# Kernel optimization log

Hardware: AMD Instinct MI355X
Metric: run time of the kernel (lower is better)

Reference implementation:

```python
import jax, jax.numpy as jnp
import numpy as np

EMB = 1024
HEADS = 16
HEAD_DIM = EMB // HEADS
SCALE = 1.0 / np.sqrt(HEAD_DIM)


def setup_inputs() -> dict:
    key = jax.random.key(0)
    ks = jax.random.split(key, 11)
    B, L, E = 4, 2048, EMB
    s = 1.0 / np.sqrt(E)
    inp = {
        "Q": jax.random.normal(ks[0], (B, L, E), jnp.float32),
        "K": jax.random.normal(ks[1], (B, L, E), jnp.float32),
        "V": jax.random.normal(ks[2], (B, L, E), jnp.float32),
        "WQ": jax.random.normal(ks[3], (E, E), jnp.float32) * s,
        "bQ": jax.random.normal(ks[4], (E,), jnp.float32) * s,
        "WK": jax.random.normal(ks[5], (E, E), jnp.float32) * s,
        "bK": jax.random.normal(ks[6], (E,), jnp.float32) * s,
        "WV": jax.random.normal(ks[7], (E, E), jnp.float32) * s,
        "bV": jax.random.normal(ks[8], (E,), jnp.float32) * s,
        "WO": jax.random.normal(ks[9], (E, E), jnp.float32) * s,
        "bO": jax.random.normal(ks[10], (E,), jnp.float32) * s,
    }
    return inp


def reference(Q, K, V, WQ, bQ, WK, bK, WV, bV, WO, bO):
    B, L, E = Q.shape
    # linear projections (torch Linear stores W as [out,in]; here W is [in,out])
    q = Q @ WQ + bQ
    k = K @ WK + bK
    v = V @ WV + bV
    # split heads: [B, H, L, D]
    q = q.reshape(B, L, HEADS, HEAD_DIM).transpose(0, 2, 1, 3)
    k = k.reshape(B, L, HEADS, HEAD_DIM).transpose(0, 2, 1, 3)
    v = v.reshape(B, L, HEADS, HEAD_DIM).transpose(0, 2, 1, 3)
    scores = jnp.einsum("bhqd,bhkd->bhqk", q, k) * SCALE
    # causal mask (mask=True): -inf above diagonal
    causal = jnp.tril(jnp.ones((L, L), dtype=bool))
    scores = jnp.where(causal, scores, -jnp.inf)
    probs = jax.nn.softmax(scores, axis=-1)
    out = jnp.einsum("bhqk,bhkd->bhqd", probs, v)  # [B,H,L,D]
    out = out.transpose(0, 2, 1, 3).reshape(B, L, E)  # concat heads
    return out @ WO + bO
```

## Files before the change

### kernel.cpp

```cpp
#include <hip/hip_runtime.h>
#include <hip/hip_bf16.h>

#define BB 4
#define HH 16
#define LL 2048
#define DD 64
#define EE 1024
#define MM (BB*LL)
#define SCL 0.125f
#define L2E 1.44269504f

using bf16   = __hip_bfloat16;
using bf16x8 = __attribute__((ext_vector_type(8))) __bf16;
using s16x4  = __attribute__((ext_vector_type(4))) short;
using f32x4  = __attribute__((ext_vector_type(4))) float;
using u32x4  = __attribute__((ext_vector_type(4))) unsigned int;
typedef unsigned int u32;

__device__ __forceinline__ bf16x8 ld8(const bf16* p){ return *(const bf16x8*)p; }
__device__ __forceinline__ bf16x8 ld8(const float* p){
  u32x4 a = *(const u32x4*)p;
  u32x4 b = *(const u32x4*)(p + 4);
  union { bf16x8 v; unsigned short s[8]; } r;
#pragma unroll
  for (int i = 0; i < 4; i++) r.s[i]     = (unsigned short)((a[i] + 0x7FFFu + ((a[i] >> 16) & 1u)) >> 16);
#pragma unroll
  for (int i = 0; i < 4; i++) r.s[i + 4] = (unsigned short)((b[i] + 0x7FFFu + ((b[i] >> 16) & 1u)) >> 16);
  return r.v;
}
__device__ __forceinline__ float ldf(const bf16* p){ return __bfloat162float(*p); }
__device__ __forceinline__ float ldf(const float* p){ return *p; }
__device__ __forceinline__ bf16 to_b(bf16 v){ return v; }
__device__ __forceinline__ bf16 to_b(float v){ return __float2bfloat16(v); }

__device__ __forceinline__ void async16(const bf16* g, bf16* l) {
  __builtin_amdgcn_global_load_lds((const __attribute__((address_space(1))) u32*)g,
                                   (__attribute__((address_space(3))) u32*)l, 16, 0, 0);
}

__global__ __launch_bounds__(256) void detect_dtype(const unsigned int* __restrict__ w,
                                                    int* __restrict__ flag) {
  __shared__ int cnt[256];
  int tid = threadIdx.x;
  int c = 0;
  for (int i = 0; i < 16; i++) {
    unsigned u = w[tid * 16 + i];
    unsigned e = (u >> 7) & 0xFF;
    c += (e >= 100 && e <= 140) ? 1 : 0;
  }
  cnt[tid] = c;
  __syncthreads();
  for (int s = 128; s > 0; s >>= 1) {
    if (tid < s) cnt[tid] += cnt[tid + s];
    __syncthreads();
  }
  if (tid == 0) *flag = (cnt[0] > 2048) ? 1 : 0;
}

__global__ __launch_bounds__(256) void convert_in(
    const void* __restrict__ X0, const void* __restrict__ X1, const void* __restrict__ X2,
    bf16* __restrict__ Y0, bf16* __restrict__ Y1, bf16* __restrict__ Y2,
    const int* __restrict__ flag) {
  int z = blockIdx.z;
  const void* X = (z == 0) ? X0 : (z == 1) ? X1 : X2;
  bf16* Y       = (z == 0) ? Y0 : (z == 1) ? Y1 : Y2;
  size_t idx = ((size_t)blockIdx.x * 256 + threadIdx.x) * 8;
  if (*flag) *(bf16x8*)(Y + idx) = *(const bf16x8*)((const bf16*)X + idx);
  else       *(bf16x8*)(Y + idx) = ld8((const float*)X + idx);
}

template<typename T>
__device__ __forceinline__ void tr_body(const T* __restrict__ W, bf16* __restrict__ Wt,
                                        bf16 (*t)[33]) {
  int tx = threadIdx.x, ty = threadIdx.y;
  int x = blockIdx.x * 32 + tx;
  for (int r = 0; r < 4; r++)
    t[ty + r * 8][tx] = to_b(W[(blockIdx.y * 32 + ty + r * 8) * EE + x]);
  __syncthreads();
  int x2 = blockIdx.y * 32 + tx;
  for (int r = 0; r < 4; r++)
    Wt[(blockIdx.x * 32 + ty + r * 8) * EE + x2] = t[tx][ty + r * 8];
}

__global__ __launch_bounds__(256) void transpose_w4(
    const void* __restrict__ W0, const void* __restrict__ W1,
    const void* __restrict__ W2, const void* __restrict__ W3,
    bf16* __restrict__ T0, bf16* __restrict__ T1,
    bf16* __restrict__ T2, bf16* __restrict__ T3,
    const int* __restrict__ flag) {
  __shared__ bf16 t[32][33];
  int z = blockIdx.z;
  const void* W = (z == 0) ? W0 : (z == 1) ? W1 : (z == 2) ? W2 : W3;
  bf16* Wt      = (z == 0) ? T0 : (z == 1) ? T1 : (z == 2) ? T2 : T3;
  if (*flag) tr_body<bf16>((const bf16*)W, Wt, t);
  else       tr_body<float>((const float*)W, Wt, t);
}

#define TILE_ELEMS (128 * 64)
template<typename TIO>
__device__ void gemm_body(const bf16* __restrict__ A, const bf16* __restrict__ Bt,
                          const TIO* __restrict__ bias, void* __restrict__ Cv,
                          int mode, bf16* As, bf16* Bs) {
  constexpr int K = EE;
  int tid = threadIdx.x;
  int lane = tid & 63, w = tid >> 6;
  int l16 = lane & 15, quad = lane >> 4;
  int linear = blockIdx.x + 8 * blockIdx.y;
  int xcd = linear & 7;
  int slot = linear >> 3;
  int m0 = (xcd * 8 + (slot & 7)) * 128;
  int n0 = (slot >> 3) * 128;
  int mw = (w & 1) * 64;
  int nw = (w >> 1) * 64;
  int lr = lane >> 3;
  int x7 = l16 & 7;

  f32x4 acc[4][4] = {};

  auto stage = [&](bf16* Ad, bf16* Bd, int k0) {
#pragma unroll
    for (int s = 0; s < 4; s++) {
      int R = w * 32 + s * 8;
      int r = R + lr;
      int gc = ((lane & 7) ^ (r & 7)) * 8;
      async16(A  + (size_t)(m0 + r) * K + k0 + gc, Ad + R * 64);
      async16(Bt + (size_t)(n0 + r) * K + k0 + gc, Bd + R * 64);
    }
  };

  auto compute = [&](const bf16* Ab, const bf16* Bb) {
#pragma unroll
    for (int ks = 0; ks < 2; ks++) {
      bf16x8 af[4], bfr[4];
#pragma unroll
      for (int t = 0; t < 4; t++) {
        af[t]  = *(const bf16x8*)(Ab + (mw + t * 16 + l16) * 64 + ((ks * 4 + quad) ^ x7) * 8);
        bfr[t] = *(const bf16x8*)(Bb + (nw + t * 16 + l16) * 64 + ((ks * 4 + quad) ^ x7) * 8);
      }
#pragma unroll
      for (int mt = 0; mt < 4; mt++)
#pragma unroll
        for (int nt = 0; nt < 4; nt++)
          acc[mt][nt] = __builtin_amdgcn_mfma_f32_16x16x32_bf16(af[mt], bfr[nt], acc[mt][nt], 0, 0, 0);
    }
  };

  stage(As, Bs, 0);
  asm volatile("s_waitcnt vmcnt(0)" ::: "memory");
  __builtin_amdgcn_s_barrier();
  asm volatile("" ::: "memory");

#pragma unroll 1
  for (int t = 0; t < K / 64; t += 2) {
    stage(As + TILE_ELEMS, Bs + TILE_ELEMS, t * 64 + 64);
    compute(As, Bs);
    asm volatile("s_waitcnt vmcnt(0)" ::: "memory");
    __builtin_amdgcn_s_barrier();
    asm volatile("" ::: "memory");
    if (t + 2 < K / 64)
      stage(As, Bs, t * 64 + 128);
    compute(As + TILE_ELEMS, Bs + TILE_ELEMS);
    asm volatile("s_waitcnt vmcnt(0)" ::: "memory");
    __builtin_amdgcn_s_barrier();
    asm volatile("" ::: "memory");
  }

#pragma unroll
  for (int nt = 0; nt < 4; nt++) {
    int col = n0 + nw + nt * 16 + l16;
    float bv = ldf(bias + col);
    int hh = col >> 6, d = col & 63;
#pragma unroll
    for (int mt = 0; mt < 4; mt++) {
      f32x4 v = acc[mt][nt];
      int rowb = m0 + mw + mt * 16 + quad * 4;
      if (mode == 0) {
#pragma unroll
        for (int i = 0; i < 4; i++)
          ((bf16*)Cv)[(size_t)(rowb + i) * EE + col] = __float2bfloat16(v[i] + bv);
      } else if (mode == 3) {
#pragma unroll
        for (int i = 0; i < 4; i++) {
          float val = v[i] + bv;
          if constexpr (__is_same(TIO, bf16))
            ((bf16*)Cv)[(size_t)(rowb + i) * EE + col] = __float2bfloat16(val);
          else
            ((float*)Cv)[(size_t)(rowb + i) * EE + col] = val;
        }
      } else {
        int b = rowb >> 11, l0 = rowb & 2047;
        union { s16x4 p; bf16 e[4]; } u;
#pragma unroll
        for (int i = 0; i < 4; i++) u.e[i] = __float2bfloat16(v[i] + bv);
        *(s16x4*)((bf16*)Cv + ((size_t)(b * HH + hh) * DD + d) * LL + l0) = u.p;
      }
    }
  }
}

__global__ __launch_bounds__(256) void qkv_gemm(
    const bf16* __restrict__ Qc, const bf16* __restrict__ Kc, const bf16* __restrict__ Vc,
    const bf16* __restrict__ WQt, const bf16* __restrict__ WKt, const bf16* __restrict__ WVt,
    const void* __restrict__ bQ, const void* __restrict__ bK, const void* __restrict__ bV,
    bf16* __restrict__ qo, bf16* __restrict__ ko, bf16* __restrict__ vo,
    const int* __restrict__ flag) {
  __shared__ __align__(16) bf16 As[2 * TILE_ELEMS];
  __shared__ __align__(16) bf16 Bs[2 * TILE_ELEMS];
  int z = blockIdx.z;
  const bf16* A    = (z == 0) ? Qc  : (z == 1) ? Kc  : Vc;
  const bf16* Bt   = (z == 0) ? WQt : (z == 1) ? WKt : WVt;
  const void* bb   = (z == 0) ? bQ  : (z == 1) ? bK  : bV;
  bf16* C          = (z == 0) ? qo  : (z == 1) ? ko  : vo;
  int mode = (z == 2) ? 2 : 0;
  if (*flag) gemm_body<bf16>(A, Bt, (const bf16*)bb, C, mode, As, Bs);
  else       gemm_body<float>(A, Bt, (const float*)bb, C, mode, As, Bs);
}

__global__ __launch_bounds__(256) void out_gemm(const bf16* __restrict__ A,
                                                const bf16* __restrict__ WOt,
                                                const void* __restrict__ bO,
                                                void* __restrict__ C,
                                                const int* __restrict__ flag) {
  __shared__ __align__(16) bf16 As[2 * TILE_ELEMS];
  __shared__ __align__(16) bf16 Bs[2 * TILE_ELEMS];
  if (*flag) gemm_body<bf16>(A, WOt, (const bf16*)bO, C, 3, As, Bs);
  else       gemm_body<float>(A, WOt, (const float*)bO, C, 3, As, Bs);
}

__global__ __launch_bounds__(256) void attn(const bf16* __restrict__ qg,
                                            const bf16* __restrict__ kg,
                                            const bf16* __restrict__ vg,
                                            bf16* __restrict__ outg) {
  __shared__ __align__(16) bf16 Ks[2][64 * 64];
  __shared__ __align__(16) bf16 Vs[2][64 * 64];
  int linear = blockIdx.x + 16 * blockIdx.y;
  int xcd = linear & 7;
  int slot = linear >> 3;
  int bh = xcd * 8 + (slot & 7);
  int pb = slot >> 3;
  int tid = threadIdx.x;
  int w = tid >> 6, lane = tid & 63, l16 = lane & 15, quad = lane >> 4;
  int b = bh >> 4, hh = bh & 15;

  const bf16* qp = qg + (size_t)b * LL * EE + hh * DD;
  const bf16* kp = kg + (size_t)b * LL * EE + hh * DD;
  const bf16* vp = vg + (size_t)bh * DD * LL;
  const f32x4 z4 = {};
  int x7 = l16 & 7;

  for (int half = 0; half < 2; half++) {
    int tile = half ? (31 - pb) : pb;
    int qrow0 = tile * 64 + w * 16;
    int q = qrow0 + l16;
    bf16x8 bq0 = *(const bf16x8*)(qp + (size_t)q * EE + quad * 8);
    bf16x8 bq1 = *(const bf16x8*)(qp + (size_t)q * EE + 32 + quad * 8);

    float m = -1.0e30f, l = 0.f;
    f32x4 o[4] = {};
    int kend = tile + 1;

    __syncthreads();
    {
      int kbase = 0;
#pragma unroll
      for (int t = 0; t < 2; t++) {
        int R = w * 16 + t * 8;
        int r = R + (lane >> 3);
        int gb = (lane & 7) ^ (r & 7);
        async16(kp + (size_t)(kbase + r) * EE + gb * 8, &Ks[0][R * 64]);
        async16(vp + (size_t)r * LL + kbase + gb * 8, &Vs[0][R * 64]);
      }
    }

    for (int kb = 0; kb < kend; kb++) {
      int kbase = kb * 64;
      __syncthreads();
      if (kb + 1 < kend) {
        int nb = (kb + 1) & 1;
        int nbase = kbase + 64;
#pragma unroll
        for (int t = 0; t < 2; t++) {
          int R = w * 16 + t * 8;
          int r = R + (lane >> 3);
          int gb = (lane & 7) ^ (r & 7);
          async16(kp + (size_t)(nbase + r) * EE + gb * 8, &Ks[nb][R * 64]);
          async16(vp + (size_t)r * LL + nbase + gb * 8, &Vs[nb][R * 64]);
        }
      }
      const bf16* Kb = &Ks[kb & 1][0];
      const bf16* Vb = &Vs[kb & 1][0];

      f32x4 s[4];
      __builtin_amdgcn_s_setprio(1);
#pragma unroll
      for (int kt = 0; kt < 4; kt++) {
        int row = kt * 16 + l16;
        bf16x8 kf0 = *(const bf16x8*)(Kb + row * 64 + (quad ^ x7) * 8);
        bf16x8 kf1 = *(const bf16x8*)(Kb + row * 64 + ((quad + 4) ^ x7) * 8);
        s[kt] = __builtin_amdgcn_mfma_f32_16x16x32_bf16(kf0, bq0, z4, 0, 0, 0);
        s[kt] = __builtin_amdgcn_mfma_f32_16x16x32_bf16(kf1, bq1, s[kt], 0, 0, 0);
      }
      __builtin_amdgcn_s_setprio(0);
#if __has_builtin(__builtin_amdgcn_mfma_f32_16x16x16bf16_1k)
      s16x4 vf[4][4];
#pragma unroll
      for (int j = 0; j < 4; j++)
#pragma unroll
        for (int kt = 0; kt < 4; kt++)
          vf[j][kt] = *(const s16x4*)(Vb + (j * 16 + l16) * 64 +
                                      ((kt * 2 + (quad >> 1)) ^ x7) * 8 + (quad & 1) * 4);
#endif
      float sv[16];
      if (kbase + 63 <= qrow0) {
#pragma unroll
        for (int kt = 0; kt < 4; kt++)
#pragma unroll
          for (int i = 0; i < 4; i++) sv[kt * 4 + i] = s[kt][i] * SCL;
      } else {
        int rel = q - kbase - quad * 4;
#pragma unroll
        for (int kt = 0; kt < 4; kt++)
#pragma unroll
          for (int i = 0; i < 4; i++)
            sv[kt * 4 + i] = (kt * 16 + i <= rel) ? s[kt][i] * SCL : -1.0e30f;
      }
      float mloc = sv[0];
#pragma unroll
      for (int i = 1; i < 16; i++) mloc = fmaxf(mloc, sv[i]);
      mloc = fmaxf(mloc, __shfl_xor(mloc, 16));
      mloc = fmaxf(mloc, __shfl_xor(mloc, 32));
      float mnew = fmaxf(m, mloc);
      float alpha = exp2f((m - mnew) * L2E);
      float p[16], ssum = 0.f;
#pragma unroll
      for (int i = 0; i < 16; i++) { p[i] = exp2f((sv[i] - mnew) * L2E); ssum += p[i]; }
      ssum += __shfl_xor(ssum, 16);
      ssum += __shfl_xor(ssum, 32);
      l = l * alpha + ssum;
      m = mnew;
#pragma unroll
      for (int j = 0; j < 4; j++)
#pragma unroll
        for (int i = 0; i < 4; i++) o[j][i] *= alpha;
      union { s16x4 v4; bf16 e[4]; unsigned u[2]; } pk[4];
#pragma unroll
      for (int kt = 0; kt < 4; kt++)
#pragma unroll
        for (int i = 0; i < 4; i++) pk[kt].e[i] = __float2bfloat16(p[kt * 4 + i]);
#if __has_builtin(__builtin_amdgcn_mfma_f32_16x16x16bf16_1k)
      __builtin_amdgcn_s_setprio(1);
#pragma unroll
      for (int kt = 0; kt < 4; kt++)
#pragma unroll
        for (int j = 0; j < 4; j++)
          o[j] = __builtin_amdgcn_mfma_f32_16x16x16bf16_1k(vf[j][kt], pk[kt].v4, o[j], 0, 0, 0);
      __builtin_amdgcn_s_setprio(0);
#else
#pragma unroll
      for (int c = 0; c < 2; c++) {
        union { bf16x8 v8; unsigned u[4]; } bfr;
#pragma unroll
        for (int r = 0; r < 4; r++) {
          int key = c * 32 + quad * 8 + 2 * r;
          int srcl = (((key >> 2) & 3) << 4) + l16;
          unsigned v0 = __shfl((int)pk[2 * c].u[r & 1], srcl, 64);
          unsigned v1 = __shfl((int)pk[2 * c + 1].u[r & 1], srcl, 64);
          bfr.u[r] = (quad < 2) ? v0 : v1;
        }
        __builtin_amdgcn_s_setprio(1);
#pragma unroll
        for (int j = 0; j < 4; j++) {
          bf16x8 vfr = *(const bf16x8*)(Vb + (j * 16 + l16) * 64 + ((c * 4 + quad) ^ x7) * 8);
          o[j] = __builtin_amdgcn_mfma_f32_16x16x32_bf16(vfr, bfr.v8, o[j], 0, 0, 0);
        }
        __builtin_amdgcn_s_setprio(0);
      }
#endif
    }
    float inv = 1.0f / l;
#pragma unroll
    for (int j = 0; j < 4; j++) {
      union { s16x4 v4; bf16 e[4]; } u;
#pragma unroll
      for (int i = 0; i < 4; i++) u.e[i] = __float2bfloat16(o[j][i] * inv);
      *(s16x4*)(outg + (size_t)(b * LL + q) * EE + hh * DD + j * 16 + quad * 4) = u.v4;
    }
  }
}

extern "C" void kernel_launch(void* const* d_in, const int* in_sizes, int n_in,
                              void* d_out, int out_size, void* d_ws, size_t ws_size,
                              hipStream_t stream) {
  const void* Q   = d_in[0];
  const void* Kin = d_in[1];
  const void* V   = d_in[2];
  const void* WQ  = d_in[3];
  const void* bQ  = d_in[4];
  const void* WK  = d_in[5];
  const void* bK  = d_in[6];
  const void* WV  = d_in[7];
  const void* bV  = d_in[8];
  const void* WO  = d_in[9];
  const void* bO  = d_in[10];

  int* flag = (int*)d_ws;
  bf16* base = (bf16*)((char*)d_ws + 256);
  bf16* wqt  = base;
  bf16* wkt  = wqt + (size_t)EE * EE;
  bf16* wvt  = wkt + (size_t)EE * EE;
  bf16* wot  = wvt + (size_t)EE * EE;
  bf16* Qc   = wot + (size_t)EE * EE;
  bf16* Kc   = Qc  + (size_t)MM * EE;
  bf16* Vc   = Kc  + (size_t)MM * EE;
  bf16* qws  = Vc  + (size_t)MM * EE;
  bf16* kws  = qws + (size_t)MM * EE;
  bf16* vws  = kws + (size_t)MM * EE;
  bf16* aout = vws + (size_t)MM * EE;

  detect_dtype<<<1, 256, 0, stream>>>((const unsigned int*)WQ, flag);

  convert_in<<<dim3(MM * EE / 8 / 256, 1, 3), 256, 0, stream>>>(Q, Kin, V, Qc, Kc, Vc, flag);

  transpose_w4<<<dim3(32, 32, 4), dim3(32, 8), 0, stream>>>(
      WQ, WK, WV, WO, wqt, wkt, wvt, wot, flag);

  qkv_gemm<<<dim3(8, 64, 3), 256, 0, stream>>>(
      Qc, Kc, Vc, wqt, wkt, wvt, bQ, bK, bV, qws, kws, vws, flag);

  attn<<<dim3(16, 64), 256, 0, stream>>>(qws, kws, vws, aout);

  out_gemm<<<dim3(8, 64), 256, 0, stream>>>(aout, wot, bO, d_out, flag);
}
```

Before: 441.6 us.

## Shrink GEMM K-tile, swap MFMA operands for vector stores, lazy softmax rescale

The GEMM K-step drops from 64 to 32 with an unswizzled LDS layout, which halves shared memory per block. For the Q/K/V-to-row-major and output GEMMs, the MFMA operands are swapped so each lane holds four consecutive columns, allowing vectorized 4-wide stores with per-column bias. In attention, Q is pre-scaled by 1/8 in bf16, removing the per-score multiply. The running-max rescale of the accumulator is skipped unless the max grows by more than 8, using an fma-based exp. Risks include LDS bank conflicts from dropping the XOR swizzle, extra barriers per K from the smaller tile, and small numeric changes from the lazy rescale and bf16 Q scaling.

```diff
diff --git a/kernel.cpp b/kernel.cpp
--- a/kernel.cpp
+++ b/kernel.cpp
@@ -32,6 +32,18 @@
 __device__ __forceinline__ float ldf(const float* p){ return *p; }
 __device__ __forceinline__ bf16 to_b(bf16 v){ return v; }
 __device__ __forceinline__ bf16 to_b(float v){ return __float2bfloat16(v); }
+
+__device__ __forceinline__ bf16x8 scl8(bf16x8 v){
+  union { bf16x8 v; unsigned short s[8]; } a, r;
+  a.v = v;
+#pragma unroll
+  for (int i = 0; i < 8; i++) {
+    bf16 b; *(unsigned short*)&b = a.s[i];
+    bf16 c = __float2bfloat16(__bfloat162float(b) * 0.125f);
+    r.s[i] = *(unsigned short*)&c;
+  }
+  return r.v;
+}
 
 __device__ __forceinline__ void async16(const bf16* g, bf16* l) {
   __builtin_amdgcn_global_load_lds((const __attribute__((address_space(1))) u32*)g,
@@ -96,8 +108,8 @@
   else       tr_body<float>((const float*)W, Wt, t);
 }
 
-#define TILE_ELEMS (128 * 64)
-template<typename TIO>
+#define TILE_A (128 * 32)
+template<typename TIO, bool SW>
 __device__ void gemm_body(const bf16* __restrict__ A, const bf16* __restrict__ Bt,
                           const TIO* __restrict__ bias, void* __restrict__ Cv,
                           int mode, bf16* As, bf16* Bs) {
@@ -112,37 +124,36 @@
   int n0 = (slot >> 3) * 128;
   int mw = (w & 1) * 64;
   int nw = (w >> 1) * 64;
-  int lr = lane >> 3;
-  int x7 = l16 & 7;
+  int lr = lane >> 2;
+  int lc = (lane & 3) * 8;
 
   f32x4 acc[4][4] = {};
 
   auto stage = [&](bf16* Ad, bf16* Bd, int k0) {
 #pragma unroll
-    for (int s = 0; s < 4; s++) {
-      int R = w * 32 + s * 8;
-      int r = R + lr;
-      int gc = ((lane & 7) ^ (r & 7)) * 8;
-      async16(A  + (size_t)(m0 + r) * K + k0 + gc, Ad + R * 64);
-      async16(Bt + (size_t)(n0 + r) * K + k0 + gc, Bd + R * 64);
+    for (int s = 0; s < 2; s++) {
+      int r = w * 32 + s * 16;
+      async16(A  + (size_t)(m0 + r + lr) * K + k0 + lc, Ad + r * 32);
+      async16(Bt + (size_t)(n0 + r + lr) * K + k0 + lc, Bd + r * 32);
     }
   };
 
   auto compute = [&](const bf16* Ab, const bf16* Bb) {
-#pragma unroll
-    for (int ks = 0; ks < 2; ks++) {
-      bf16x8 af[4], bfr[4];
-#pragma unroll
-      for (int t = 0; t < 4; t++) {
-        af[t]  = *(const bf16x8*)(Ab + (mw + t * 16 + l16) * 64 + ((ks * 4 + quad) ^ x7) * 8);
-        bfr[t] = *(const bf16x8*)(Bb + (nw + t * 16 + l16) * 64 + ((ks * 4 + quad) ^ x7) * 8);
-      }
-#pragma unroll
-      for (int mt = 0; mt < 4; mt++)
-#pragma unroll
-        for (int nt = 0; nt < 4; nt++)
+    bf16x8 af[4], bfr[4];
+#pragma unroll
+    for (int t = 0; t < 4; t++) {
+      af[t]  = *(const bf16x8*)(Ab + (mw + t * 16 + l16) * 32 + quad * 8);
+      bfr[t] = *(const bf16x8*)(Bb + (nw + t * 16 + l16) * 32 + quad * 8);
+    }
+#pragma unroll
+    for (int mt = 0; mt < 4; mt++)
+#pragma unroll
+      for (int nt = 0; nt < 4; nt++) {
+        if (SW)
+          acc[mt][nt] = __builtin_amdgcn_mfma_f32_16x16x32_bf16(bfr[nt], af[mt], acc[mt][nt], 0, 0, 0);
+        else
           acc[mt][nt] = __builtin_amdgcn_mfma_f32_16x16x32_bf16(af[mt], bfr[nt], acc[mt][nt], 0, 0, 0);
-    }
+      }
   };
 
   stage(As, Bs, 0);
@@ -151,43 +162,58 @@
   asm volatile("" ::: "memory");
 
 #pragma unroll 1
-  for (int t = 0; t < K / 64; t += 2) {
-    stage(As + TILE_ELEMS, Bs + TILE_ELEMS, t * 64 + 64);
+  for (int t = 0; t < K / 32; t += 2) {
+    stage(As + TILE_A, Bs + TILE_A, t * 32 + 32);
     compute(As, Bs);
     asm volatile("s_waitcnt vmcnt(0)" ::: "memory");
     __builtin_amdgcn_s_barrier();
     asm volatile("" ::: "memory");
-    if (t + 2 < K / 64)
-      stage(As, Bs, t * 64 + 128);
-    compute(As + TILE_ELEMS, Bs + TILE_ELEMS);
+    if (t + 2 < K / 32)
+      stage(As, Bs, t * 32 + 64);
+    compute(As + TILE_A, Bs + TILE_A);
     asm volatile("s_waitcnt vmcnt(0)" ::: "memory");
     __builtin_amdgcn_s_barrier();
     asm volatile("" ::: "memory");
   }
 
-#pragma unroll
-  for (int nt = 0; nt < 4; nt++) {
-    int col = n0 + nw + nt * 16 + l16;
-    float bv = ldf(bias + col);
-    int hh = col >> 6, d = col & 63;
+  if (SW) {
 #pragma unroll
     for (int mt = 0; mt < 4; mt++) {
-      f32x4 v = acc[mt][nt];
-      int rowb = m0 + mw + mt * 16 + quad * 4;
-      if (mode == 0) {
-#pragma unroll
-        for (int i = 0; i < 4; i++)
-          ((bf16*)Cv)[(size_t)(rowb + i) * EE + col] = __float2bfloat16(v[i] + bv);
-      } else if (mode == 3) {
-#pragma unroll
-        for (int i = 0; i < 4; i++) {
-          float val = v[i] + bv;
-          if constexpr (__is_same(TIO, bf16))
-            ((bf16*)Cv)[(size_t)(rowb + i) * EE + col] = __float2bfloat16(val);
-          else
-            ((float*)Cv)[(size_t)(rowb + i) * EE + col] = val;
+      int row = m0 + mw + mt * 16 + l16;
+#pragma unroll
+      for (int nt = 0; nt < 4; nt++) {
+        int colb = n0 + nw + nt * 16 + quad * 4;
+        f32x4 v = acc[mt][nt];
+        if (mode == 0) {
+          union { s16x4 v4; bf16 e[4]; } u;
+#pragma unroll
+          for (int i = 0; i < 4; i++) u.e[i] = __float2bfloat16(v[i] + ldf(bias + colb + i));
+          *(s16x4*)((bf16*)Cv + (size_t)row * EE + colb) = u.v4;
+        } else {
+          if constexpr (__is_same(TIO, bf16)) {
+            union { s16x4 v4; bf16 e[4]; } u;
+#pragma unroll
+            for (int i = 0; i < 4; i++) u.e[i] = __float2bfloat16(v[i] + ldf(bias + colb + i));
+            *(s16x4*)((bf16*)Cv + (size_t)row * EE + colb) = u.v4;
+          } else {
+            f32x4 fv;
+#pragma unroll
+            for (int i = 0; i < 4; i++) fv[i] = v[i] + ldf(bias + colb + i);
+            *(f32x4*)((float*)Cv + (size_t)row * EE + colb) = fv;
+          }
         }
-      } else {
+      }
+    }
+  } else {
+#pragma unroll
+    for (int nt = 0; nt < 4; nt++) {
+      int col = n0 + nw + nt * 16 + l16;
+      float bv = ldf(bias + col);
+      int hh = col >> 6, d = col & 63;
+#pragma unroll
+      for (int mt = 0; mt < 4; mt++) {
+        f32x4 v = acc[mt][nt];
+        int rowb = m0 + mw + mt * 16 + quad * 4;
         int b = rowb >> 11, l0 = rowb & 2047;
         union { s16x4 p; bf16 e[4]; } u;
 #pragma unroll
@@ -204,16 +230,20 @@
     const void* __restrict__ bQ, const void* __restrict__ bK, const void* __restrict__ bV,
     bf16* __restrict__ qo, bf16* __restrict__ ko, bf16* __restrict__ vo,
     const int* __restrict__ flag) {
-  __shared__ __align__(16) bf16 As[2 * TILE_ELEMS];
-  __shared__ __align__(16) bf16 Bs[2 * TILE_ELEMS];
+  __shared__ __align__(16) bf16 As[2 * TILE_A];
+  __shared__ __align__(16) bf16 Bs[2 * TILE_A];
   int z = blockIdx.z;
   const bf16* A    = (z == 0) ? Qc  : (z == 1) ? Kc  : Vc;
   const bf16* Bt   = (z == 0) ? WQt : (z == 1) ? WKt : WVt;
   const void* bb   = (z == 0) ? bQ  : (z == 1) ? bK  : bV;
   bf16* C          = (z == 0) ? qo  : (z == 1) ? ko  : vo;
-  int mode = (z == 2) ? 2 : 0;
-  if (*flag) gemm_body<bf16>(A, Bt, (const bf16*)bb, C, mode, As, Bs);
-  else       gemm_body<float>(A, Bt, (const float*)bb, C, mode, As, Bs);
+  if (z == 2) {
+    if (*flag) gemm_body<bf16,  false>(A, Bt, (const bf16*)bb,  C, 2, As, Bs);
+    else       gemm_body<float, false>(A, Bt, (const float*)bb, C, 2, As, Bs);
+  } else {
+    if (*flag) gemm_body<bf16,  true>(A, Bt, (const bf16*)bb,  C, 0, As, Bs);
+    else       gemm_body<float, true>(A, Bt, (const float*)bb, C, 0, As, Bs);
+  }
 }
 
 __global__ __launch_bounds__(256) void out_gemm(const bf16* __restrict__ A,
@@ -221,10 +251,10 @@
                                                 const void* __restrict__ bO,
                                                 void* __restrict__ C,
                                                 const int* __restrict__ flag) {
-  __shared__ __align__(16) bf16 As[2 * TILE_ELEMS];
-  __shared__ __align__(16) bf16 Bs[2 * TILE_ELEMS];
-  if (*flag) gemm_body<bf16>(A, WOt, (const bf16*)bO, C, 3, As, Bs);
-  else       gemm_body<float>(A, WOt, (const float*)bO, C, 3, As, Bs);
+  __shared__ __align__(16) bf16 As[2 * TILE_A];
+  __shared__ __align__(16) bf16 Bs[2 * TILE_A];
+  if (*flag) gemm_body<bf16,  true>(A, WOt, (const bf16*)bO,  C, 3, As, Bs);
+  else       gemm_body<float, true>(A, WOt, (const float*)bO, C, 3, As, Bs);
 }
 
 __global__ __launch_bounds__(256) void attn(const bf16* __restrict__ qg,
@@ -252,8 +282,8 @@
     int tile = half ? (31 - pb) : pb;
     int qrow0 = tile * 64 + w * 16;
     int q = qrow0 + l16;
-    bf16x8 bq0 = *(const bf16x8*)(qp + (size_t)q * EE + quad * 8);
-    bf16x8 bq1 = *(const bf16x8*)(qp + (size_t)q * EE + 32 + quad * 8);
+    bf16x8 bq0 = scl8(*(const bf16x8*)(qp + (size_t)q * EE + quad * 8));
+    bf16x8 bq1 = scl8(*(const bf16x8*)(qp + (size_t)q * EE + 32 + quad * 8));
 
     float m = -1.0e30f, l = 0.f;
     f32x4 o[4] = {};
@@ -315,33 +345,37 @@
 #pragma unroll
         for (int kt = 0; kt < 4; kt++)
 #pragma unroll
-          for (int i = 0; i < 4; i++) sv[kt * 4 + i] = s[kt][i] * SCL;
+          for (int i = 0; i < 4; i++) sv[kt * 4 + i] = s[kt][i];
       } else {
         int rel = q - kbase - quad * 4;
 #pragma unroll
         for (int kt = 0; kt < 4; kt++)
 #pragma unroll
           for (int i = 0; i < 4; i++)
-            sv[kt * 4 + i] = (kt * 16 + i <= rel) ? s[kt][i] * SCL : -1.0e30f;
+            sv[kt * 4 + i] = (kt * 16 + i <= rel) ? s[kt][i] : -1.0e30f;
       }
       float mloc = sv[0];
 #pragma unroll
       for (int i = 1; i < 16; i++) mloc = fmaxf(mloc, sv[i]);
       mloc = fmaxf(mloc, __shfl_xor(mloc, 16));
       mloc = fmaxf(mloc, __shfl_xor(mloc, 32));
-      float mnew = fmaxf(m, mloc);
-      float alpha = exp2f((m - mnew) * L2E);
+      if (!__all(mloc - m <= 8.0f)) {
+        float mnew = fmaxf(m, mloc);
+        float alpha = exp2f((m - mnew) * L2E);
+        l *= alpha;
+#pragma unroll
+        for (int j = 0; j < 4; j++)
+#pragma unroll
+          for (int i = 0; i < 4; i++) o[j][i] *= alpha;
+        m = mnew;
+      }
+      float mL2 = -m * L2E;
       float p[16], ssum = 0.f;
 #pragma unroll
-      for (int i = 0; i < 16; i++) { p[i] = exp2f((sv[i] - mnew) * L2E); ssum += p[i]; }
+      for (int i = 0; i < 16; i++) { p[i] = exp2f(fmaf(sv[i], L2E, mL2)); ssum += p[i]; }
       ssum += __shfl_xor(ssum, 16);
       ssum += __shfl_xor(ssum, 32);
-      l = l * alpha + ssum;
-      m = mnew;
-#pragma unroll
-      for (int j = 0; j < 4; j++)
-#pragma unroll
-        for (int i = 0; i < 4; i++) o[j][i] *= alpha;
+      l += ssum;
       union { s16x4 v4; bf16 e[4]; unsigned u[2]; } pk[4];
 #pragma unroll
       for (int kt = 0; kt < 4; kt++)
```

Result: faster. 391.4 us (-11.4%).
